# Kernel tuning notes

Measured on AMD Instinct MI355X. Metric: run time of the kernel, lower is better.

## Reference

```python
import jax, jax.numpy as jnp
import numpy as np
import math

B, S, N, D, H = 4, 64, 256, 512, 8
DEPTH = D // H

def setup_inputs() -> dict:
    key = jax.random.key(0)
    ks = jax.random.split(key, 9)
    scale = 1.0 / math.sqrt(D)
    return {
        "x": jax.random.normal(ks[0], (B, S, N, D), dtype=jnp.float32),
        "Wq": jax.random.normal(ks[1], (D, D), dtype=jnp.float32) * scale,
        "bq": jax.random.normal(ks[2], (D,), dtype=jnp.float32) * 0.01,
        "Wk": jax.random.normal(ks[3], (D, D), dtype=jnp.float32) * scale,
        "bk": jax.random.normal(ks[4], (D,), dtype=jnp.float32) * 0.01,
        "Wv": jax.random.normal(ks[5], (D, D), dtype=jnp.float32) * scale,
        "bv": jax.random.normal(ks[6], (D,), dtype=jnp.float32) * 0.01,
        "Wo": jax.random.normal(ks[7], (D, D), dtype=jnp.float32) * scale,
        "bo": jax.random.normal(ks[8], (D,), dtype=jnp.float32) * 0.01,
    }

def _split_heads(t):
    # (B, S, M, D) -> (B, H, S, M, depth); matches split_head.forward (4D path)
    # followed by the att_dim==2 permute(0, 2, 1, 3, 4) in cross_attention.
    b, s, m, _ = t.shape
    return t.reshape(b, s, m, H, DEPTH).transpose(0, 3, 1, 2, 4)

def reference(x, Wq, bq, Wk, bk, Wv, bv, Wo, bo):
    b, s, n, d = x.shape
    # att_dim == 2: query is the cls token along the joint/patch axis.
    q = _split_heads(x[:, :, 0:1, :] @ Wq + bq)   # (B, H, S, 1, depth)
    k = _split_heads(x @ Wk + bk)                  # (B, H, S, N, depth)
    v = _split_heads(x @ Wv + bv)                  # (B, H, S, N, depth)
    # scaled dot product attention (mask is None in cross_attention)
    logits = jnp.einsum('bhsqd,bhskd->bhsqk', q, k) / math.sqrt(DEPTH)
    attn = jax.nn.softmax(logits, axis=-1)         # (B, H, S, 1, N)
    ctx = jnp.einsum('bhsqk,bhskd->bhsqd', attn, v)  # (B, H, S, 1, depth)
    # permute(0, 2, 3, 1, 4) then reshape (B, S, 1, D)
    concat = ctx.transpose(0, 2, 3, 1, 4).reshape(b, s, 1, d)
    return concat @ Wo + bo
```

## Files before the change

kernel.cpp:

```cpp
#include <hip/hip_runtime.h>
#include <stdint.h>
#include <math.h>


#define NT 16

__global__ __launch_bounds__(1024, 4) void fused_kernel(
    const float* __restrict__ x,
    const float* __restrict__ Wq, const float* __restrict__ bq,
    const float* __restrict__ Wk,
    const float* __restrict__ Wv, const float* __restrict__ bv,
    const float* __restrict__ Wo, const float* __restrict__ bo,
    float* __restrict__ out) {
  const int bs = blockIdx.x;
  const int t = threadIdx.x;
  const int w = t >> 6, lane = t & 63;
  const float* xb = x + (long)bs * 131072;

  __shared__ float q_s[512], x0_s[512], ctx_s[512];
  __shared__ float r_s[4096];
  __shared__ float red_s[7][512];
  __shared__ float ypar[8][512];
  __shared__ float y_sp[8][520];
  __shared__ float pt_s[2][8][NT];
  __shared__ float f_s[2][8];
  __shared__ float s_s[8];

  const int hg = w & 1;
  const int rw = w >> 1;

  if (t < 128) *(float4*)&x0_s[t * 4] = *(const float4*)&xb[t * 4];
  float4 c00 = *(const float4*)&xb[(long)rw * 512 + lane * 8];
  float4 c01 = *(const float4*)&xb[(long)rw * 512 + lane * 8 + 4];
  float4 c10 = *(const float4*)&xb[(long)(8 + rw) * 512 + lane * 8];
  float4 c11 = *(const float4*)&xb[(long)(8 + rw) * 512 + lane * 8 + 4];
  __syncthreads();

  {
    const int j4 = (t & 127) * 4;
    const int kq = t >> 7;
    float4 a = make_float4(0.f, 0.f, 0.f, 0.f);
    const float* wp = Wq + (long)(kq * 64) * 512 + j4;
    const float* ap = &x0_s[kq * 64];
#pragma unroll 8
    for (int k = 0; k < 64; ++k) {
      float4 wv = *(const float4*)&wp[(long)k * 512];
      float av = ap[k];
      a.x += av * wv.x; a.y += av * wv.y; a.z += av * wv.z; a.w += av * wv.w;
    }
    if (kq > 0) *(float4*)&red_s[kq - 1][j4] = a;
    __syncthreads();
    if (kq == 0) {
#pragma unroll
      for (int rr = 0; rr < 7; ++rr) {
        float4 b = *(const float4*)&red_s[rr][j4];
        a.x += b.x; a.y += b.y; a.z += b.z; a.w += b.w;
      }
      float4 bb = *(const float4*)&bq[j4];
      a.x += bb.x; a.y += bb.y; a.z += bb.z; a.w += bb.w;
      *(float4*)&q_s[j4] = a;
    }
  }
  __syncthreads();

  {
    const int d = t >> 1, hh = t & 1;
    const float* wrow = Wk + (long)d * 512 + hh * 256;
#pragma unroll
    for (int hi = 0; hi < 4; ++hi) {
      const int h = hh * 4 + hi;
      const float* qp = &q_s[h * 64];
      float racc = 0.f;
#pragma unroll
      for (int c4 = 0; c4 < 16; ++c4) {
        float4 wv = *(const float4*)&wrow[hi * 64 + c4 * 4];
        racc += qp[c4 * 4 + 0] * wv.x + qp[c4 * 4 + 1] * wv.y +
                qp[c4 * 4 + 2] * wv.z + qp[c4 * 4 + 3] * wv.w;
      }
      r_s[h * 512 + d] = racc;
    }
  }
  __syncthreads();

  float rv[4][8];
#pragma unroll
  for (int hi = 0; hi < 4; ++hi) {
    const int h = hg * 4 + hi;
    float4 a = *(const float4*)&r_s[h * 512 + lane * 8];
    float4 b = *(const float4*)&r_s[h * 512 + lane * 8 + 4];
    rv[hi][0] = a.x; rv[hi][1] = a.y; rv[hi][2] = a.z; rv[hi][3] = a.w;
    rv[hi][4] = b.x; rv[hi][5] = b.y; rv[hi][6] = b.z; rv[hi][7] = b.w;
  }

  float accy[8] = {0.f, 0.f, 0.f, 0.f, 0.f, 0.f, 0.f, 0.f};
  float m_h = -INFINITY, s_h = 0.f;
  const int dcol = t & 511, halfn = t >> 9;

  for (int tile = 0; tile < 16; ++tile) {
    const int b = tile & 1;

    {
      float acc[4];
#pragma unroll
      for (int hi = 0; hi < 4; ++hi)
        acc[hi] = c00.x * rv[hi][0] + c00.y * rv[hi][1] + c00.z * rv[hi][2] + c00.w * rv[hi][3]
                + c01.x * rv[hi][4] + c01.y * rv[hi][5] + c01.z * rv[hi][6] + c01.w * rv[hi][7];
#pragma unroll
      for (int j = 0; j < 2; ++j) {
        float v = (lane & 2) ? acc[j] : acc[j + 2];
        float tt = __shfl_xor(v, 2);
        acc[j] = ((lane & 2) ? acc[j + 2] : acc[j]) + tt;
      }
      {
        float v = (lane & 1) ? acc[0] : acc[1];
        float tt = __shfl_xor(v, 1);
        acc[0] = ((lane & 1) ? acc[1] : acc[0]) + tt;
      }
      acc[0] += __shfl_xor(acc[0], 4);
      acc[0] += __shfl_xor(acc[0], 8);
      acc[0] += __shfl_xor(acc[0], 16);
      acc[0] += __shfl_xor(acc[0], 32);
      if (lane < 4) pt_s[b][hg * 4 + lane][rw] = acc[0] * 0.125f;
#pragma unroll
      for (int hi = 0; hi < 4; ++hi)
        acc[hi] = c10.x * rv[hi][0] + c10.y * rv[hi][1] + c10.z * rv[hi][2] + c10.w * rv[hi][3]
                + c11.x * rv[hi][4] + c11.y * rv[hi][5] + c11.z * rv[hi][6] + c11.w * rv[hi][7];
#pragma unroll
      for (int j = 0; j < 2; ++j) {
        float v = (lane & 2) ? acc[j] : acc[j + 2];
        float tt = __shfl_xor(v, 2);
        acc[j] = ((lane & 2) ? acc[j + 2] : acc[j]) + tt;
      }
      {
        float v = (lane & 1) ? acc[0] : acc[1];
        float tt = __shfl_xor(v, 1);
        acc[0] = ((lane & 1) ? acc[1] : acc[0]) + tt;
      }
      acc[0] += __shfl_xor(acc[0], 4);
      acc[0] += __shfl_xor(acc[0], 8);
      acc[0] += __shfl_xor(acc[0], 16);
      acc[0] += __shfl_xor(acc[0], 32);
      if (lane < 4) pt_s[b][hg * 4 + lane][8 + rw] = acc[0] * 0.125f;
    }
    __syncthreads();

    if (w < 8) {
      float l = (lane < 16) ? pt_s[b][w][lane] : -3.0e38f;
      float tm = l;
#pragma unroll
      for (int o = 8; o; o >>= 1) tm = fmaxf(tm, __shfl_xor(tm, o));
      float m_new = fmaxf(m_h, tm);
      float e = __expf(l - m_new);
      float ts = e;
#pragma unroll
      for (int o = 8; o; o >>= 1) ts += __shfl_xor(ts, o);
      float f = __expf(m_h - m_new);
      s_h = s_h * f + ts;
      m_h = m_new;
      if (lane == 0) f_s[b][w] = f;
      if (lane < 16) pt_s[b][w][lane] = e;
    }
    __syncthreads();

    float4 n00, n01, n10, n11;
    if (tile < 15) {
      const float* nx = xb + (long)(tile + 1) * 8192;
      n00 = *(const float4*)&nx[(long)rw * 512 + lane * 8];
      n01 = *(const float4*)&nx[(long)rw * 512 + lane * 8 + 4];
      n10 = *(const float4*)&nx[(long)(8 + rw) * 512 + lane * 8];
      n11 = *(const float4*)&nx[(long)(8 + rw) * 512 + lane * 8 + 4];
    }

    {
#pragma unroll
      for (int h = 0; h < 8; ++h) accy[h] *= f_s[b][h];
      const float* xg = xb + ((long)tile * 16 + halfn * 8) * 512 + dcol;
#pragma unroll
      for (int n4 = 0; n4 < 2; ++n4) {
        const int nb = halfn * 8 + n4 * 4;
        float xv0 = xg[(long)(n4 * 4 + 0) * 512];
        float xv1 = xg[(long)(n4 * 4 + 1) * 512];
        float xv2 = xg[(long)(n4 * 4 + 2) * 512];
        float xv3 = xg[(long)(n4 * 4 + 3) * 512];
#pragma unroll
        for (int h = 0; h < 8; ++h) {
          float4 p4 = *(const float4*)&pt_s[b][h][nb];
          accy[h] += p4.x * xv0 + p4.y * xv1 + p4.z * xv2 + p4.w * xv3;
        }
      }
    }
    if (tile < 15) { c00 = n00; c01 = n01; c10 = n10; c11 = n11; }
  }

  if (w < 8 && lane == 0) s_s[w] = s_h;
  __syncthreads();
  if (halfn == 1) {
#pragma unroll
    for (int h = 0; h < 8; ++h) ypar[h][dcol] = accy[h];
  }
  __syncthreads();
  if (halfn == 0) {
#pragma unroll
    for (int h = 0; h < 8; ++h)
      y_sp[h][dcol] = (accy[h] + ypar[h][dcol]) * (1.f / s_s[h]);
  }
  __syncthreads();

  {
    const int o4 = (t & 127) * 4;
    const int kq = t >> 7;
    const int h0 = o4 >> 6;
    float4 a = make_float4(0.f, 0.f, 0.f, 0.f);
    const float* wp = Wv + (long)(kq * 64) * 512 + o4;
    const float* yp2 = &y_sp[h0][kq * 64];
#pragma unroll 8
    for (int k = 0; k < 64; ++k) {
      float4 wv = *(const float4*)&wp[(long)k * 512];
      float yv = yp2[k];
      a.x += yv * wv.x; a.y += yv * wv.y; a.z += yv * wv.z; a.w += yv * wv.w;
    }
    if (kq > 0) *(float4*)&red_s[kq - 1][o4] = a;
    __syncthreads();
    if (kq == 0) {
#pragma unroll
      for (int rr = 0; rr < 7; ++rr) {
        float4 b = *(const float4*)&red_s[rr][o4];
        a.x += b.x; a.y += b.y; a.z += b.z; a.w += b.w;
      }
      float4 bb = *(const float4*)&bv[o4];
      a.x += bb.x; a.y += bb.y; a.z += bb.z; a.w += bb.w;
      *(float4*)&ctx_s[o4] = a;
    }
  }
  __syncthreads();

  {
    const int j4 = (t & 127) * 4;
    const int kq = t >> 7;
    float4 a = make_float4(0.f, 0.f, 0.f, 0.f);
    const float* wp = Wo + (long)(kq * 64) * 512 + j4;
    const float* cp = &ctx_s[kq * 64];
#pragma unroll 8
    for (int k = 0; k < 64; ++k) {
      float4 wv = *(const float4*)&wp[(long)k * 512];
      float cv = cp[k];
      a.x += cv * wv.x; a.y += cv * wv.y; a.z += cv * wv.z; a.w += cv * wv.w;
    }
    if (kq > 0) *(float4*)&red_s[kq - 1][j4] = a;
    __syncthreads();
    if (kq == 0) {
#pragma unroll
      for (int rr = 0; rr < 7; ++rr) {
        float4 b = *(const float4*)&red_s[rr][j4];
        a.x += b.x; a.y += b.y; a.z += b.z; a.w += b.w;
      }
      float4 bb = *(const float4*)&bo[j4];
      a.x += bb.x; a.y += bb.y; a.z += bb.z; a.w += bb.w;
      *(float4*)&out[(long)bs * 512 + j4] = a;
    }
  }
}

extern "C" void kernel_launch(void* const* d_in, const int* in_sizes, int n_in,
                              void* d_out, int out_size, void* d_ws, size_t ws_size,
                              hipStream_t stream) {
  (void)in_sizes; (void)n_in; (void)out_size; (void)d_ws; (void)ws_size;
  const float* x  = (const float*)d_in[0];
  const float* Wq = (const float*)d_in[1];
  const float* bq = (const float*)d_in[2];
  const float* Wk = (const float*)d_in[3];
  const float* Wv = (const float*)d_in[5];
  const float* bv = (const float*)d_in[6];
  const float* Wo = (const float*)d_in[7];
  const float* bo = (const float*)d_in[8];
  float* out = (float*)d_out;

  fused_kernel<<<256, 1024, 0, stream>>>(x, Wq, bq, Wk, Wv, bv, Wo, bo, out);
}
```

Measured before the change: 296.4 us.

## Split fused kernel by head group and move output projection to batched GEMM

The single 256-block, 1024-thread kernel is split into 512 blocks of 512 threads, with each block handling one (batch,seq) row and one half of the heads. This doubles grid parallelism across the CUs and removes the cross-half reduction of the attention context. The output projection is moved into a separate small GEMM kernel that batches 4 rows per block, so Wo loads are shared across rows. In exchange, each x row is now streamed twice (once per head group), Wq and Wk are partially recomputed, and there is an extra launch plus a workspace round trip.

```diff
diff --git a/kernel.cpp b/kernel.cpp
--- a/kernel.cpp
+++ b/kernel.cpp
@@ -3,42 +3,38 @@
 #include <math.h>
 
 
-#define NT 16
-
-__global__ __launch_bounds__(1024, 4) void fused_kernel(
+__global__ __launch_bounds__(512, 4) void fused_half(
     const float* __restrict__ x,
     const float* __restrict__ Wq, const float* __restrict__ bq,
     const float* __restrict__ Wk,
     const float* __restrict__ Wv, const float* __restrict__ bv,
-    const float* __restrict__ Wo, const float* __restrict__ bo,
-    float* __restrict__ out) {
-  const int bs = blockIdx.x;
+    float* __restrict__ ctx_ws) {
+  const int bs = blockIdx.x >> 1;
+  const int hg = blockIdx.x & 1;
   const int t = threadIdx.x;
   const int w = t >> 6, lane = t & 63;
   const float* xb = x + (long)bs * 131072;
 
-  __shared__ float q_s[512], x0_s[512], ctx_s[512];
-  __shared__ float r_s[4096];
-  __shared__ float red_s[7][512];
-  __shared__ float ypar[8][512];
-  __shared__ float y_sp[8][520];
-  __shared__ float pt_s[2][8][NT];
-  __shared__ float f_s[2][8];
-  __shared__ float s_s[8];
-
-  const int hg = w & 1;
-  const int rw = w >> 1;
+  __shared__ __align__(16) float x0_s[512];
+  __shared__ __align__(16) float q_s[256];
+  __shared__ __align__(16) float r_s[4 * 512];
+  __shared__ __align__(16) float red_s[7][256];
+  __shared__ __align__(16) float y_sp[4][520];
+  __shared__ __align__(16) float pt_s[2][4][16];
+  __shared__ float f_s[2][4];
+  __shared__ float s_s[4];
 
   if (t < 128) *(float4*)&x0_s[t * 4] = *(const float4*)&xb[t * 4];
-  float4 c00 = *(const float4*)&xb[(long)rw * 512 + lane * 8];
-  float4 c01 = *(const float4*)&xb[(long)rw * 512 + lane * 8 + 4];
-  float4 c10 = *(const float4*)&xb[(long)(8 + rw) * 512 + lane * 8];
-  float4 c11 = *(const float4*)&xb[(long)(8 + rw) * 512 + lane * 8 + 4];
+  float4 c00 = *(const float4*)&xb[(long)w * 512 + lane * 8];
+  float4 c01 = *(const float4*)&xb[(long)w * 512 + lane * 8 + 4];
+  float4 c10 = *(const float4*)&xb[(long)(8 + w) * 512 + lane * 8];
+  float4 c11 = *(const float4*)&xb[(long)(8 + w) * 512 + lane * 8 + 4];
   __syncthreads();
 
   {
-    const int j4 = (t & 127) * 4;
-    const int kq = t >> 7;
+    const int jj = t & 63;
+    const int kq = t >> 6;
+    const int j4 = hg * 256 + jj * 4;
     float4 a = make_float4(0.f, 0.f, 0.f, 0.f);
     const float* wp = Wq + (long)(kq * 64) * 512 + j4;
     const float* ap = &x0_s[kq * 64];
@@ -48,53 +44,50 @@
       float av = ap[k];
       a.x += av * wv.x; a.y += av * wv.y; a.z += av * wv.z; a.w += av * wv.w;
     }
-    if (kq > 0) *(float4*)&red_s[kq - 1][j4] = a;
+    if (kq > 0) *(float4*)&red_s[kq - 1][jj * 4] = a;
     __syncthreads();
     if (kq == 0) {
 #pragma unroll
       for (int rr = 0; rr < 7; ++rr) {
-        float4 b = *(const float4*)&red_s[rr][j4];
+        float4 b = *(const float4*)&red_s[rr][jj * 4];
         a.x += b.x; a.y += b.y; a.z += b.z; a.w += b.w;
       }
       float4 bb = *(const float4*)&bq[j4];
       a.x += bb.x; a.y += bb.y; a.z += bb.z; a.w += bb.w;
-      *(float4*)&q_s[j4] = a;
+      *(float4*)&q_s[jj * 4] = a;
     }
   }
   __syncthreads();
 
   {
-    const int d = t >> 1, hh = t & 1;
-    const float* wrow = Wk + (long)d * 512 + hh * 256;
-#pragma unroll
-    for (int hi = 0; hi < 4; ++hi) {
-      const int h = hh * 4 + hi;
-      const float* qp = &q_s[h * 64];
+    const int d = t;
+    const float* wrow = Wk + (long)d * 512 + hg * 256;
+#pragma unroll
+    for (int hl = 0; hl < 4; ++hl) {
+      const float* qp = &q_s[hl * 64];
       float racc = 0.f;
 #pragma unroll
       for (int c4 = 0; c4 < 16; ++c4) {
-        float4 wv = *(const float4*)&wrow[hi * 64 + c4 * 4];
+        float4 wv = *(const float4*)&wrow[hl * 64 + c4 * 4];
         racc += qp[c4 * 4 + 0] * wv.x + qp[c4 * 4 + 1] * wv.y +
                 qp[c4 * 4 + 2] * wv.z + qp[c4 * 4 + 3] * wv.w;
       }
-      r_s[h * 512 + d] = racc;
+      r_s[hl * 512 + d] = racc;
     }
   }
   __syncthreads();
 
   float rv[4][8];
 #pragma unroll
-  for (int hi = 0; hi < 4; ++hi) {
-    const int h = hg * 4 + hi;
-    float4 a = *(const float4*)&r_s[h * 512 + lane * 8];
-    float4 b = *(const float4*)&r_s[h * 512 + lane * 8 + 4];
-    rv[hi][0] = a.x; rv[hi][1] = a.y; rv[hi][2] = a.z; rv[hi][3] = a.w;
-    rv[hi][4] = b.x; rv[hi][5] = b.y; rv[hi][6] = b.z; rv[hi][7] = b.w;
-  }
-
-  float accy[8] = {0.f, 0.f, 0.f, 0.f, 0.f, 0.f, 0.f, 0.f};
+  for (int hl = 0; hl < 4; ++hl) {
+    float4 a = *(const float4*)&r_s[hl * 512 + lane * 8];
+    float4 b = *(const float4*)&r_s[hl * 512 + lane * 8 + 4];
+    rv[hl][0] = a.x; rv[hl][1] = a.y; rv[hl][2] = a.z; rv[hl][3] = a.w;
+    rv[hl][4] = b.x; rv[hl][5] = b.y; rv[hl][6] = b.z; rv[hl][7] = b.w;
+  }
+
+  float accy[4] = {0.f, 0.f, 0.f, 0.f};
   float m_h = -INFINITY, s_h = 0.f;
-  const int dcol = t & 511, halfn = t >> 9;
 
   for (int tile = 0; tile < 16; ++tile) {
     const int b = tile & 1;
@@ -102,9 +95,9 @@
     {
       float acc[4];
 #pragma unroll
-      for (int hi = 0; hi < 4; ++hi)
-        acc[hi] = c00.x * rv[hi][0] + c00.y * rv[hi][1] + c00.z * rv[hi][2] + c00.w * rv[hi][3]
-                + c01.x * rv[hi][4] + c01.y * rv[hi][5] + c01.z * rv[hi][6] + c01.w * rv[hi][7];
+      for (int hl = 0; hl < 4; ++hl)
+        acc[hl] = c00.x * rv[hl][0] + c00.y * rv[hl][1] + c00.z * rv[hl][2] + c00.w * rv[hl][3]
+                + c01.x * rv[hl][4] + c01.y * rv[hl][5] + c01.z * rv[hl][6] + c01.w * rv[hl][7];
 #pragma unroll
       for (int j = 0; j < 2; ++j) {
         float v = (lane & 2) ? acc[j] : acc[j + 2];
@@ -120,11 +113,11 @@
       acc[0] += __shfl_xor(acc[0], 8);
       acc[0] += __shfl_xor(acc[0], 16);
       acc[0] += __shfl_xor(acc[0], 32);
-      if (lane < 4) pt_s[b][hg * 4 + lane][rw] = acc[0] * 0.125f;
-#pragma unroll
-      for (int hi = 0; hi < 4; ++hi)
-        acc[hi] = c10.x * rv[hi][0] + c10.y * rv[hi][1] + c10.z * rv[hi][2] + c10.w * rv[hi][3]
-                + c11.x * rv[hi][4] + c11.y * rv[hi][5] + c11.z * rv[hi][6] + c11.w * rv[hi][7];
+      if (lane < 4) pt_s[b][lane][w] = acc[0] * 0.125f;
+#pragma unroll
+      for (int hl = 0; hl < 4; ++hl)
+        acc[hl] = c10.x * rv[hl][0] + c10.y * rv[hl][1] + c10.z * rv[hl][2] + c10.w * rv[hl][3]
+                + c11.x * rv[hl][4] + c11.y * rv[hl][5] + c11.z * rv[hl][6] + c11.w * rv[hl][7];
 #pragma unroll
       for (int j = 0; j < 2; ++j) {
         float v = (lane & 2) ? acc[j] : acc[j + 2];
@@ -140,11 +133,11 @@
       acc[0] += __shfl_xor(acc[0], 8);
       acc[0] += __shfl_xor(acc[0], 16);
       acc[0] += __shfl_xor(acc[0], 32);
-      if (lane < 4) pt_s[b][hg * 4 + lane][8 + rw] = acc[0] * 0.125f;
-    }
-    __syncthreads();
-
-    if (w < 8) {
+      if (lane < 4) pt_s[b][lane][8 + w] = acc[0] * 0.125f;
+    }
+    __syncthreads();
+
+    if (w < 4) {
       float l = (lane < 16) ? pt_s[b][w][lane] : -3.0e38f;
       float tm = l;
 #pragma unroll
@@ -165,106 +158,126 @@
     float4 n00, n01, n10, n11;
     if (tile < 15) {
       const float* nx = xb + (long)(tile + 1) * 8192;
-      n00 = *(const float4*)&nx[(long)rw * 512 + lane * 8];
-      n01 = *(const float4*)&nx[(long)rw * 512 + lane * 8 + 4];
-      n10 = *(const float4*)&nx[(long)(8 + rw) * 512 + lane * 8];
-      n11 = *(const float4*)&nx[(long)(8 + rw) * 512 + lane * 8 + 4];
+      n00 = *(const float4*)&nx[(long)w * 512 + lane * 8];
+      n01 = *(const float4*)&nx[(long)w * 512 + lane * 8 + 4];
+      n10 = *(const float4*)&nx[(long)(8 + w) * 512 + lane * 8];
+      n11 = *(const float4*)&nx[(long)(8 + w) * 512 + lane * 8 + 4];
     }
 
     {
 #pragma unroll
-      for (int h = 0; h < 8; ++h) accy[h] *= f_s[b][h];
-      const float* xg = xb + ((long)tile * 16 + halfn * 8) * 512 + dcol;
-#pragma unroll
-      for (int n4 = 0; n4 < 2; ++n4) {
-        const int nb = halfn * 8 + n4 * 4;
+      for (int hl = 0; hl < 4; ++hl) accy[hl] *= f_s[b][hl];
+      const float* xg = xb + (long)tile * 8192 + t;
+#pragma unroll
+      for (int n4 = 0; n4 < 4; ++n4) {
         float xv0 = xg[(long)(n4 * 4 + 0) * 512];
         float xv1 = xg[(long)(n4 * 4 + 1) * 512];
         float xv2 = xg[(long)(n4 * 4 + 2) * 512];
         float xv3 = xg[(long)(n4 * 4 + 3) * 512];
 #pragma unroll
-        for (int h = 0; h < 8; ++h) {
-          float4 p4 = *(const float4*)&pt_s[b][h][nb];
-          accy[h] += p4.x * xv0 + p4.y * xv1 + p4.z * xv2 + p4.w * xv3;
+        for (int hl = 0; hl < 4; ++hl) {
+          float4 p4 = *(const float4*)&pt_s[b][hl][n4 * 4];
+          accy[hl] += p4.x * xv0 + p4.y * xv1 + p4.z * xv2 + p4.w * xv3;
         }
       }
     }
     if (tile < 15) { c00 = n00; c01 = n01; c10 = n10; c11 = n11; }
   }
 
-  if (w < 8 && lane == 0) s_s[w] = s_h;
-  __syncthreads();
-  if (halfn == 1) {
-#pragma unroll
-    for (int h = 0; h < 8; ++h) ypar[h][dcol] = accy[h];
-  }
-  __syncthreads();
-  if (halfn == 0) {
-#pragma unroll
-    for (int h = 0; h < 8; ++h)
-      y_sp[h][dcol] = (accy[h] + ypar[h][dcol]) * (1.f / s_s[h]);
-  }
+  if (w < 4 && lane == 0) s_s[w] = s_h;
+  __syncthreads();
+#pragma unroll
+  for (int hl = 0; hl < 4; ++hl)
+    y_sp[hl][t] = accy[hl] * (1.f / s_s[hl]);
   __syncthreads();
 
   {
-    const int o4 = (t & 127) * 4;
-    const int kq = t >> 7;
-    const int h0 = o4 >> 6;
+    const int jj = t & 63;
+    const int kq = t >> 6;
+    const int o4 = hg * 256 + jj * 4;
+    const int hl = jj >> 4;
     float4 a = make_float4(0.f, 0.f, 0.f, 0.f);
     const float* wp = Wv + (long)(kq * 64) * 512 + o4;
-    const float* yp2 = &y_sp[h0][kq * 64];
+    const float* yp = &y_sp[hl][kq * 64];
 #pragma unroll 8
     for (int k = 0; k < 64; ++k) {
       float4 wv = *(const float4*)&wp[(long)k * 512];
-      float yv = yp2[k];
+      float yv = yp[k];
       a.x += yv * wv.x; a.y += yv * wv.y; a.z += yv * wv.z; a.w += yv * wv.w;
     }
-    if (kq > 0) *(float4*)&red_s[kq - 1][o4] = a;
+    if (kq > 0) *(float4*)&red_s[kq - 1][jj * 4] = a;
     __syncthreads();
     if (kq == 0) {
 #pragma unroll
       for (int rr = 0; rr < 7; ++rr) {
-        float4 b = *(const float4*)&red_s[rr][o4];
+        float4 b = *(const float4*)&red_s[rr][jj * 4];
         a.x += b.x; a.y += b.y; a.z += b.z; a.w += b.w;
       }
       float4 bb = *(const float4*)&bv[o4];
       a.x += bb.x; a.y += bb.y; a.z += bb.z; a.w += bb.w;
-      *(float4*)&ctx_s[o4] = a;
-    }
-  }
-  __syncthreads();
-
-  {
-    const int j4 = (t & 127) * 4;
-    const int kq = t >> 7;
-    float4 a = make_float4(0.f, 0.f, 0.f, 0.f);
-    const float* wp = Wo + (long)(kq * 64) * 512 + j4;
-    const float* cp = &ctx_s[kq * 64];
+      *(float4*)&ctx_ws[(long)bs * 512 + o4] = a;
+    }
+  }
+}
+
+__global__ __launch_bounds__(256) void gemm_ks_kernel(
+    const float* __restrict__ A, const float* __restrict__ W,
+    const float* __restrict__ bias, float* __restrict__ C) {
+  __shared__ float a_s[4][512];
+  __shared__ float red_s[3][4][64];
+  const int rt = blockIdx.x, jt = blockIdx.y, t = threadIdx.x;
+  const int w = t >> 6, lane = t & 63;
+
+#pragma unroll
+  for (int l = 0; l < 2; ++l) {
+    int flat4 = t + l * 256;
+    int arow = flat4 >> 7;
+    int k4 = (flat4 & 127) * 4;
+    float4 v = *(const float4*)&A[(long)(rt * 4 + arow) * 512 + k4];
+    a_s[arow][k4] = v.x; a_s[arow][k4 + 1] = v.y;
+    a_s[arow][k4 + 2] = v.z; a_s[arow][k4 + 3] = v.w;
+  }
+  __syncthreads();
+
+  const int j = jt * 64 + lane;
+  float acc0 = 0.f, acc1 = 0.f, acc2 = 0.f, acc3 = 0.f;
+  const float* wp = W + (long)(w * 128) * 512 + j;
+  const float* ap = &a_s[0][w * 128];
 #pragma unroll 8
-    for (int k = 0; k < 64; ++k) {
-      float4 wv = *(const float4*)&wp[(long)k * 512];
-      float cv = cp[k];
-      a.x += cv * wv.x; a.y += cv * wv.y; a.z += cv * wv.z; a.w += cv * wv.w;
-    }
-    if (kq > 0) *(float4*)&red_s[kq - 1][j4] = a;
-    __syncthreads();
-    if (kq == 0) {
-#pragma unroll
-      for (int rr = 0; rr < 7; ++rr) {
-        float4 b = *(const float4*)&red_s[rr][j4];
-        a.x += b.x; a.y += b.y; a.z += b.z; a.w += b.w;
-      }
-      float4 bb = *(const float4*)&bo[j4];
-      a.x += bb.x; a.y += bb.y; a.z += bb.z; a.w += bb.w;
-      *(float4*)&out[(long)bs * 512 + j4] = a;
-    }
+  for (int k = 0; k < 128; ++k) {
+    float wv = wp[(long)k * 512];
+    acc0 += ap[k] * wv;
+    acc1 += ap[512 + k] * wv;
+    acc2 += ap[1024 + k] * wv;
+    acc3 += ap[1536 + k] * wv;
+  }
+  if (w > 0) {
+    red_s[w - 1][0][lane] = acc0;
+    red_s[w - 1][1][lane] = acc1;
+    red_s[w - 1][2][lane] = acc2;
+    red_s[w - 1][3][lane] = acc3;
+  }
+  __syncthreads();
+  if (w == 0) {
+#pragma unroll
+    for (int rr = 0; rr < 3; ++rr) {
+      acc0 += red_s[rr][0][lane];
+      acc1 += red_s[rr][1][lane];
+      acc2 += red_s[rr][2][lane];
+      acc3 += red_s[rr][3][lane];
+    }
+    const float b = bias[j];
+    C[(long)(rt * 4 + 0) * 512 + j] = acc0 + b;
+    C[(long)(rt * 4 + 1) * 512 + j] = acc1 + b;
+    C[(long)(rt * 4 + 2) * 512 + j] = acc2 + b;
+    C[(long)(rt * 4 + 3) * 512 + j] = acc3 + b;
   }
 }
 
 extern "C" void kernel_launch(void* const* d_in, const int* in_sizes, int n_in,
                               void* d_out, int out_size, void* d_ws, size_t ws_size,
                               hipStream_t stream) {
-  (void)in_sizes; (void)n_in; (void)out_size; (void)d_ws; (void)ws_size;
+  (void)in_sizes; (void)n_in; (void)out_size; (void)ws_size;
   const float* x  = (const float*)d_in[0];
   const float* Wq = (const float*)d_in[1];
   const float* bq = (const float*)d_in[2];
@@ -274,6 +287,8 @@
   const float* Wo = (const float*)d_in[7];
   const float* bo = (const float*)d_in[8];
   float* out = (float*)d_out;
-
-  fused_kernel<<<256, 1024, 0, stream>>>(x, Wq, bq, Wk, Wv, bv, Wo, bo, out);
+  float* ctx_ws = (float*)d_ws;
+
+  fused_half<<<512, 512, 0, stream>>>(x, Wq, bq, Wk, Wv, bv, ctx_ws);
+  gemm_ks_kernel<<<dim3(64, 8), 256, 0, stream>>>(ctx_ws, Wo, bo, out);
 }
```

Result: no change. 298.5 us (+0.7%).
